# Optimization experiments

Measured on AMD Instinct MI355X. Metric: run time of the kernel, lower is better.

Reference implementation:

```python
import jax, jax.numpy as jnp
import numpy as np

N = 500000   # nodes per graph batch
E = 8000000  # edges per graph batch
B = 4096     # number of graphs
C = 2        # node feature dim
D = 2        # edge feature dim


def setup_inputs() -> dict:
    key = jax.random.key(0)
    ks = jax.random.split(key, 16)
    inp = {
        "x_a": jax.random.normal(ks[0], (N, C), jnp.float32),
        "edge_index_a": jax.random.randint(ks[1], (2, E), 0, N, jnp.int32),
        "edge_attr_a": jax.random.normal(ks[2], (E, D), jnp.float32),
        "batch_a": jnp.sort(jax.random.randint(ks[3], (N,), 0, B, jnp.int32)),
        "x_b": jax.random.normal(ks[4], (N, C), jnp.float32),
        "edge_index_b": jax.random.randint(ks[5], (2, E), 0, N, jnp.int32),
        "edge_attr_b": jax.random.normal(ks[6], (E, D), jnp.float32),
        "batch_b": jnp.sort(jax.random.randint(ks[7], (N,), 0, B, jnp.int32)),
        "targets": jax.random.normal(ks[8], (B,), jnp.float32),
        "num_graphs": B,
        # CGConv params: lin_f, lin_s each Linear(2*C+D=6 -> C)
        "Wf": jax.random.normal(ks[9], (2 * C + D, C), jnp.float32) * 0.4,
        "bf": jnp.zeros((C,), jnp.float32),
        "Ws": jax.random.normal(ks[10], (2 * C + D, C), jnp.float32) * 0.4,
        "bs": jnp.zeros((C,), jnp.float32),
        # l1: Linear(2 -> 3), l2: Linear(6 -> 1)
        "W1": jax.random.normal(ks[11], (C, 3), jnp.float32) * 0.5,
        "b1": jnp.zeros((3,), jnp.float32),
        "W2": jax.random.normal(ks[12], (6, 1), jnp.float32) * 0.4,
        "b2": jnp.zeros((1,), jnp.float32),
    }
    return inp


def cg_conv(x, edge_index, edge_attr, Wf, bf, Ws, bs):
    # PyG CGConv: out_i = x_i + sum_{j->i} sigmoid(lin_f(z)) * softplus(lin_s(z)),
    # z = [x_i, x_j, e_ij]; source_to_target flow => i = edge_index[1].
    src, dst = edge_index[0], edge_index[1]
    z = jnp.concatenate([x[dst], x[src], edge_attr], axis=1)  # [E, 6]
    m = jax.nn.sigmoid(z @ Wf + bf) * jax.nn.softplus(z @ Ws + bs)  # [E, C]
    agg = jax.ops.segment_sum(m, dst, num_segments=x.shape[0])
    return x + agg


def branch(x, edge_index, edge_attr, batch, num_graphs,
           Wf, bf, Ws, bs, W1, b1):
    h = cg_conv(x, edge_index, edge_attr, Wf, bf, Ws, bs)
    h = jax.nn.relu(h @ W1 + b1)  # [N, 3]
    sums = jax.ops.segment_sum(h, batch, num_segments=num_graphs)
    cnts = jax.ops.segment_sum(jnp.ones((h.shape[0],), h.dtype), batch,
                               num_segments=num_graphs)
    return sums / jnp.maximum(cnts, 1.0)[:, None]  # global_mean_pool [B, 3]


def reference(x_a, edge_index_a, edge_attr_a, batch_a,
              x_b, edge_index_b, edge_attr_b, batch_b,
              targets, num_graphs,
              Wf, bf, Ws, bs, W1, b1, W2, b2):
    out_1 = branch(x_a, edge_index_a, edge_attr_a, batch_a, num_graphs,
                   Wf, bf, Ws, bs, W1, b1)
    out_2 = branch(x_b, edge_index_b, edge_attr_b, batch_b, num_graphs,
                   Wf, bf, Ws, bs, W1, b1)
    out = jnp.concatenate([out_1, out_2], axis=1)  # [B, 6]
    out = jax.nn.relu(out @ W2 + b2)               # [B, 1]
    loss = jnp.mean((out[:, 0] - targets) ** 2)
    return out, loss
```

## Files before the change

### kernel.cpp

```cpp
#include <hip/hip_runtime.h>

#define N_NODES 500000
#define N_EDGES 8000000
#define N_GRAPHS 4096

#define NB 128
#define BIN_SHIFT 12
#define BIN_NODES 4096
#define NBINS 123
#define BIN_CAP 66560
#define T_EDGES 2048
#define P1_THREADS 512
#define EPT (T_EDGES / P1_THREADS)
#define P1_GRID ((N_EDGES + T_EDGES - 1) / T_EDGES)
#define K 4
#define P2_GRID (NBINS * K)
#define SLICE_F (BIN_NODES * 2)
#define FXS 131072.0f
#define FXI (1.0f / 131072.0f)
#define M_MAX 250.0f
#define OVF_CAP 8192
#define SGRID ((N_NODES + 255) / 256)

#define OFF_CURS_A   0
#define OFF_CURS_B   512
#define OFF_OVFC_A   1024
#define OFF_OVFC_B   1280
#define ZERO_SMALL   1536
#define OFF_STARTS_A 4096
#define OFF_STARTS_B 20736
#define OFF_MEAN_A   37376
#define OFF_MEAN_B   86528
#define OFF_OVF_A    135680
#define OFF_OVF_B    266752
#define OFF_SCRATCH  397824
#define OFF_BINS     16519680
#define WS_NEED      82014720ull

__device__ __forceinline__ float2 ntload_f2(const float2* p) {
    unsigned long long v = __builtin_nontemporal_load((const unsigned long long*)p);
    float2 r;
    r.x = __uint_as_float((unsigned int)v);
    r.y = __uint_as_float((unsigned int)(v >> 32));
    return r;
}

__global__ __launch_bounds__(512, 8) void p1_kernel(
    const float* __restrict__ x, const int* __restrict__ ei,
    const float* __restrict__ ea,
    const float* __restrict__ Wf, const float* __restrict__ bfv,
    const float* __restrict__ Ws, const float* __restrict__ bsv,
    unsigned long long* __restrict__ bins, unsigned int* __restrict__ cursors,
    unsigned int* __restrict__ ovf_cnt, float4* __restrict__ ovf)
{
    __shared__ unsigned long long sorted[T_EDGES];
    __shared__ unsigned int whist[8][NB];
    __shared__ unsigned int base[NB];
    __shared__ unsigned int cur[NB];
    __shared__ unsigned int gbase[NB];
    __shared__ unsigned int ntot_s;
    unsigned char* binof = (unsigned char*)whist;

    int t = threadIdx.x;
    int wave = t >> 6;
    int ebase = blockIdx.x * T_EDGES;

    for (int i = t; i < 8 * NB; i += P1_THREADS) ((unsigned int*)whist)[i] = 0;
    __syncthreads();

    int d[EPT], s[EPT];
#pragma unroll
    for (int i = 0; i < EPT; ++i) {
        int e = ebase + i * P1_THREADS + t;
        if (e < N_EDGES) {
            d[i] = __builtin_nontemporal_load(ei + N_EDGES + e);
            s[i] = __builtin_nontemporal_load(ei + e);
        } else { d[i] = -1; s[i] = 0; }
        if (d[i] >= 0)
            atomicAdd(&whist[wave][((unsigned)d[i]) >> BIN_SHIFT], 1u);
    }
    __syncthreads();

    unsigned g0 = 0, g1 = 0;
    if (t < 64) {
        unsigned tot0 = 0, tot1 = 0;
#pragma unroll
        for (int w = 0; w < 8; ++w) { tot0 += whist[w][2*t]; tot1 += whist[w][2*t+1]; }
        unsigned pair = tot0 + tot1;
        unsigned v = pair;
#pragma unroll
        for (int off = 1; off < 64; off <<= 1) {
            unsigned u = __shfl_up(v, off);
            if (t >= off) v += u;
        }
        unsigned excl = v - pair;
        base[2*t]   = excl;        cur[2*t]   = excl;
        base[2*t+1] = excl + tot0; cur[2*t+1] = excl + tot0;
        if (t == 63) ntot_s = v;
        g0 = tot0 ? atomicAdd(&cursors[2*t],   tot0) : 0u;
        g1 = tot1 ? atomicAdd(&cursors[2*t+1], tot1) : 0u;
    }
    __syncthreads();

    float2 xdv[EPT], xsv[EPT], eav[EPT];
#pragma unroll
    for (int i = 0; i < EPT; ++i) {
        int e = ebase + i * P1_THREADS + t;
        if (e < N_EDGES) {
            xdv[i] = ((const float2*)x)[d[i]];
            xsv[i] = ((const float2*)x)[s[i]];
            eav[i] = ntload_f2((const float2*)ea + e);
        }
    }

    float wf[12], wsv[12];
#pragma unroll
    for (int i = 0; i < 12; ++i) { wf[i] = Wf[i]; wsv[i] = Ws[i]; }
    float bf0 = bfv[0], bf1 = bfv[1], bs0 = bsv[0], bs1 = bsv[1];

#pragma unroll
    for (int i = 0; i < EPT; ++i) {
        int e = ebase + i * P1_THREADS + t;
        if (e >= N_EDGES) continue;
        int dst = d[i];
        float z0 = xdv[i].x, z1 = xdv[i].y;
        float z2 = xsv[i].x, z3 = xsv[i].y;
        float z4 = eav[i].x, z5 = eav[i].y;

        float f0 = bf0 + z0*wf[0] + z1*wf[2] + z2*wf[4] + z3*wf[6] + z4*wf[8]  + z5*wf[10];
        float f1 = bf1 + z0*wf[1] + z1*wf[3] + z2*wf[5] + z3*wf[7] + z4*wf[9]  + z5*wf[11];
        float s0 = bs0 + z0*wsv[0] + z1*wsv[2] + z2*wsv[4] + z3*wsv[6] + z4*wsv[8]  + z5*wsv[10];
        float s1 = bs1 + z0*wsv[1] + z1*wsv[3] + z2*wsv[5] + z3*wsv[7] + z4*wsv[9]  + z5*wsv[11];

        float m0 = (1.f/(1.f+__expf(-f0))) * (fmaxf(s0,0.f) + __logf(1.f+__expf(-fabsf(s0))));
        float m1 = (1.f/(1.f+__expf(-f1))) * (fmaxf(s1,0.f) + __logf(1.f+__expf(-fabsf(s1))));

        int b = (int)((unsigned)dst >> BIN_SHIFT);
        unsigned slot = atomicAdd(&cur[b], 1u);
        unsigned long long pk = 0ull;
        if (m0 < M_MAX && m1 < M_MAX) {
            unsigned fx0 = __float2uint_rn(m0 * FXS);
            unsigned fx1 = __float2uint_rn(m1 * FXS);
            pk = (unsigned long long)((unsigned)dst & (BIN_NODES - 1))
               | ((unsigned long long)fx0 << 12)
               | ((unsigned long long)fx1 << 37);
        } else {
            unsigned oi = atomicAdd(ovf_cnt, 1u);
            if (oi < OVF_CAP) ovf[oi] = make_float4(__int_as_float(dst), m0, m1, 0.f);
        }
        sorted[slot] = pk;
        binof[slot] = (unsigned char)b;
    }
    if (t < 64) { gbase[2*t] = g0; gbase[2*t+1] = g1; }
    __syncthreads();

    int ntot = (int)ntot_s;
    for (int p = t; p < ntot; p += P1_THREADS) {
        int lo = (int)binof[p];
        unsigned gpos = gbase[lo] + (unsigned)(p - (int)base[lo]);
        unsigned long long v = sorted[p];
        if (gpos < BIN_CAP) {
            __builtin_nontemporal_store(v, &bins[(size_t)lo * BIN_CAP + gpos]);
        } else {
            int local = (int)(v & (BIN_NODES - 1));
            float m0 = (float)((unsigned)((v >> 12) & 0x1FFFFFFu)) * FXI;
            float m1 = (float)((unsigned)((v >> 37) & 0x1FFFFFFu)) * FXI;
            int dst = (lo << BIN_SHIFT) + local;
            unsigned oi = atomicAdd(ovf_cnt, 1u);
            if (oi < OVF_CAP) ovf[oi] = make_float4(__int_as_float(dst), m0, m1, 0.f);
        }
    }
}

__global__ __launch_bounds__(512, 8) void p2_kernel(
    const unsigned long long* __restrict__ bins,
    const unsigned int* __restrict__ cursors,
    float* __restrict__ scratch)
{
    __shared__ float acc[SLICE_F];
    int b = blockIdx.x >> 2;
    int k = blockIdx.x & 3;
    int t = threadIdx.x;
#pragma unroll
    for (int i = t; i < SLICE_F; i += 512) acc[i] = 0.f;
    __syncthreads();

    int n = (int)min(cursors[b], (unsigned)BIN_CAP);
    int s = (n * k) / K, e = (n * (k + 1)) / K;
    const unsigned long long* bp = bins + (size_t)b * BIN_CAP;
    for (int i = s + t; i < e; i += 512) {
        unsigned long long v = __builtin_nontemporal_load(bp + i);
        int local = (int)(v & (BIN_NODES - 1));
        float m0 = (float)((unsigned)((v >> 12) & 0x1FFFFFFu)) * FXI;
        float m1 = (float)((unsigned)((v >> 37) & 0x1FFFFFFu)) * FXI;
        atomicAdd(&acc[local],             m0);
        atomicAdd(&acc[BIN_NODES + local], m1);
    }
    __syncthreads();

    float4* dst = (float4*)(scratch + (size_t)(b * K + k) * SLICE_F);
#pragma unroll
    for (int i = t; i < BIN_NODES / 2; i += 512) {
        float a0 = acc[2*i],             a1 = acc[2*i + 1];
        float b0 = acc[BIN_NODES + 2*i], b1 = acc[BIN_NODES + 2*i + 1];
        dst[i] = make_float4(a0, b0, a1, b1);
    }
}

__global__ __launch_bounds__(256) void ovf_kernel(
    const float4* __restrict__ ovf, const unsigned int* __restrict__ ovf_cnt,
    float* __restrict__ scratch)
{
    int n = (int)min(*ovf_cnt, (unsigned)OVF_CAP);
    for (int i = threadIdx.x; i < n; i += 256) {
        float4 r = ovf[i];
        int dst = __float_as_int(r.x);
        int b = dst >> BIN_SHIFT, local = dst & (BIN_NODES - 1);
        float* p = scratch + (size_t)(b * K) * SLICE_F + 2 * local;
        unsafeAtomicAdd(p,     r.y);
        unsafeAtomicAdd(p + 1, r.z);
    }
}

__global__ __launch_bounds__(256) void starts_kernel(
    const int* __restrict__ ba, const int* __restrict__ bb,
    unsigned int* __restrict__ sa, unsigned int* __restrict__ sb)
{
    int blk = blockIdx.x;
    const int* batch = ba;
    unsigned int* starts = sa;
    if (blk >= SGRID) { blk -= SGRID; batch = bb; starts = sb; }
    int i = blk * 256 + threadIdx.x;
    if (i >= N_NODES) return;
    int b1 = batch[i];
    if (i == 0) {
        for (int g = 0; g <= b1; ++g) starts[g] = 0;
    } else {
        int b0 = batch[i - 1];
        for (int g = b0 + 1; g <= b1; ++g) starts[g] = i;
    }
    if (i == N_NODES - 1) {
        for (int g = b1 + 1; g <= N_GRAPHS; ++g) starts[g] = N_NODES;
    }
}

__global__ __launch_bounds__(256) void pool2_kernel(
    const float* __restrict__ x, const float* __restrict__ scratch,
    const unsigned int* __restrict__ starts,
    const float* __restrict__ W1, const float* __restrict__ b1,
    float* __restrict__ mean_out)
{
    int wave = threadIdx.x >> 6, lane = threadIdx.x & 63;
    int g = blockIdx.x * 4 + wave;

    float w00 = W1[0], w01 = W1[1], w02 = W1[2];
    float w10 = W1[3], w11 = W1[4], w12 = W1[5];
    float c0 = b1[0], c1 = b1[1], c2 = b1[2];

    const float2* sc2 = (const float2*)scratch;
    int s = (int)starts[g], e = (int)starts[g + 1];
    float a0 = 0.f, a1 = 0.f, a2 = 0.f;
    for (int i = s + lane; i < e; i += 64) {
        int b = i >> BIN_SHIFT, local = i & (BIN_NODES - 1);
        size_t f2base = (size_t)(b * K) * BIN_NODES + local;
        float2 g0 = sc2[f2base];
        float2 g1 = sc2[f2base + BIN_NODES];
        float2 g2 = sc2[f2base + 2 * BIN_NODES];
        float2 g3 = sc2[f2base + 3 * BIN_NODES];
        float2 xv = ((const float2*)x)[i];
        float h0 = xv.x + g0.x + g1.x + g2.x + g3.x;
        float h1 = xv.y + g0.y + g1.y + g2.y + g3.y;
        a0 += fmaxf(h0*w00 + h1*w10 + c0, 0.f);
        a1 += fmaxf(h0*w01 + h1*w11 + c1, 0.f);
        a2 += fmaxf(h0*w02 + h1*w12 + c2, 0.f);
    }
#pragma unroll
    for (int off = 32; off; off >>= 1) {
        a0 += __shfl_down(a0, off);
        a1 += __shfl_down(a1, off);
        a2 += __shfl_down(a2, off);
    }
    if (lane == 0) {
        float inv = 1.0f / fmaxf((float)(e - s), 1.0f);
        mean_out[3*(size_t)g]     = a0 * inv;
        mean_out[3*(size_t)g + 1] = a1 * inv;
        mean_out[3*(size_t)g + 2] = a2 * inv;
    }
}

__global__ __launch_bounds__(1024) void final_kernel(
    const float* __restrict__ ma, const float* __restrict__ mb,
    const float* __restrict__ W2, const float* __restrict__ b2,
    const float* __restrict__ targets,
    float* __restrict__ out)
{
    __shared__ float red[1024];
    float w0 = W2[0], w1 = W2[1], w2 = W2[2], w3 = W2[3], w4 = W2[4], w5 = W2[5];
    float bias = b2[0];

    float lsum = 0.f;
    for (int g = threadIdx.x; g < N_GRAPHS; g += 1024) {
        float v = bias
                + ma[3*(size_t)g]*w0 + ma[3*(size_t)g+1]*w1 + ma[3*(size_t)g+2]*w2
                + mb[3*(size_t)g]*w3 + mb[3*(size_t)g+1]*w4 + mb[3*(size_t)g+2]*w5;
        v = fmaxf(v, 0.f);
        out[g] = v;
        float d = v - targets[g];
        lsum += d * d;
    }
    red[threadIdx.x] = lsum;
    __syncthreads();
#pragma unroll
    for (int off = 512; off; off >>= 1) {
        if (threadIdx.x < (unsigned)off) red[threadIdx.x] += red[threadIdx.x + off];
        __syncthreads();
    }
    if (threadIdx.x == 0) out[N_GRAPHS] = red[0] * (1.0f / (float)N_GRAPHS);
}

#define FB_SCALE 4194304.0f
#define FB_INV   2.384185791015625e-07f

__global__ __launch_bounds__(256) void fb_edge_kernel(
    const float* __restrict__ x, const int* __restrict__ ei,
    const float* __restrict__ ea,
    const float* __restrict__ Wf, const float* __restrict__ bfv,
    const float* __restrict__ Ws, const float* __restrict__ bsv,
    unsigned long long* __restrict__ agg)
{
    float wf[12], ws[12];
#pragma unroll
    for (int i = 0; i < 12; ++i) { wf[i] = Wf[i]; ws[i] = Ws[i]; }
    float bf0 = bfv[0], bf1 = bfv[1], bs0 = bsv[0], bs1 = bsv[1];

    int e = blockIdx.x * 256 + threadIdx.x;
    int src = ei[e];
    int dst = ei[N_EDGES + e];
    float2 xd = ((const float2*)x)[dst];
    float2 xs = ((const float2*)x)[src];
    float2 ev = ((const float2*)ea)[e];
    float z0 = xd.x, z1 = xd.y, z2 = xs.x, z3 = xs.y, z4 = ev.x, z5 = ev.y;

    float f0 = bf0 + z0*wf[0] + z1*wf[2] + z2*wf[4] + z3*wf[6] + z4*wf[8]  + z5*wf[10];
    float f1 = bf1 + z0*wf[1] + z1*wf[3] + z2*wf[5] + z3*wf[7] + z4*wf[9]  + z5*wf[11];
    float s0 = bs0 + z0*ws[0] + z1*ws[2] + z2*ws[4] + z3*ws[6] + z4*ws[8]  + z5*ws[10];
    float s1 = bs1 + z0*ws[1] + z1*ws[3] + z2*ws[5] + z3*ws[7] + z4*ws[9]  + z5*ws[11];

    float m0 = (1.f/(1.f+__expf(-f0))) * (fmaxf(s0,0.f) + __logf(1.f+__expf(-fabsf(s0))));
    float m1 = (1.f/(1.f+__expf(-f1))) * (fmaxf(s1,0.f) + __logf(1.f+__expf(-fabsf(s1))));

    unsigned int fx0 = __float2uint_rn(m0 * FB_SCALE);
    unsigned int fx1 = __float2uint_rn(m1 * FB_SCALE);
    atomicAdd(&agg[dst], (unsigned long long)fx0 | ((unsigned long long)fx1 << 32));
}

__global__ __launch_bounds__(64) void fb_pool_kernel(
    const float* __restrict__ x, const unsigned long long* __restrict__ agg,
    const int* __restrict__ batch,
    const float* __restrict__ W1, const float* __restrict__ b1,
    float* __restrict__ mean_out)
{
    int b = blockIdx.x;
    float w00 = W1[0], w01 = W1[1], w02 = W1[2];
    float w10 = W1[3], w11 = W1[4], w12 = W1[5];
    float c0 = b1[0], c1 = b1[1], c2 = b1[2];

    int lo = 0, hi = N_NODES;
    while (lo < hi) { int mid = (lo + hi) >> 1; if (batch[mid] < b) lo = mid + 1; else hi = mid; }
    int seg_s = lo;
    hi = N_NODES;
    while (lo < hi) { int mid = (lo + hi) >> 1; if (batch[mid] < b + 1) lo = mid + 1; else hi = mid; }
    int seg_e = lo;

    float a0 = 0.f, a1 = 0.f, a2 = 0.f;
    for (int i = seg_s + (int)threadIdx.x; i < seg_e; i += 64) {
        unsigned long long v = agg[i];
        float g0 = (float)(unsigned int)(v & 0xffffffffull) * FB_INV;
        float g1 = (float)(unsigned int)(v >> 32) * FB_INV;
        float2 xv = ((const float2*)x)[i];
        float h0 = xv.x + g0, h1 = xv.y + g1;
        a0 += fmaxf(h0*w00 + h1*w10 + c0, 0.f);
        a1 += fmaxf(h0*w01 + h1*w11 + c1, 0.f);
        a2 += fmaxf(h0*w02 + h1*w12 + c2, 0.f);
    }
#pragma unroll
    for (int off = 32; off; off >>= 1) {
        a0 += __shfl_down(a0, off);
        a1 += __shfl_down(a1, off);
        a2 += __shfl_down(a2, off);
    }
    if (threadIdx.x == 0) {
        float inv = 1.0f / fmaxf((float)(seg_e - seg_s), 1.0f);
        mean_out[3*(size_t)b]     = a0 * inv;
        mean_out[3*(size_t)b + 1] = a1 * inv;
        mean_out[3*(size_t)b + 2] = a2 * inv;
    }
}

extern "C" void kernel_launch(void* const* d_in, const int* in_sizes, int n_in,
                              void* d_out, int out_size, void* d_ws, size_t ws_size,
                              hipStream_t stream) {
    const float* x_a     = (const float*)d_in[0];
    const int*   ei_a    = (const int*)  d_in[1];
    const float* ea_a    = (const float*)d_in[2];
    const int*   batch_a = (const int*)  d_in[3];
    const float* x_b     = (const float*)d_in[4];
    const int*   ei_b    = (const int*)  d_in[5];
    const float* ea_b    = (const float*)d_in[6];
    const int*   batch_b = (const int*)  d_in[7];
    const float* targets = (const float*)d_in[8];
    const float* Wf = (const float*)d_in[10];
    const float* bf = (const float*)d_in[11];
    const float* Ws = (const float*)d_in[12];
    const float* bs = (const float*)d_in[13];
    const float* W1 = (const float*)d_in[14];
    const float* b1 = (const float*)d_in[15];
    const float* W2 = (const float*)d_in[16];
    const float* b2 = (const float*)d_in[17];
    float* out = (float*)d_out;
    char* ws = (char*)d_ws;

    if (ws_size >= WS_NEED) {
        unsigned int* curs_a   = (unsigned int*)(ws + OFF_CURS_A);
        unsigned int* curs_b   = (unsigned int*)(ws + OFF_CURS_B);
        unsigned int* ovfc_a   = (unsigned int*)(ws + OFF_OVFC_A);
        unsigned int* ovfc_b   = (unsigned int*)(ws + OFF_OVFC_B);
        unsigned int* starts_a = (unsigned int*)(ws + OFF_STARTS_A);
        unsigned int* starts_b = (unsigned int*)(ws + OFF_STARTS_B);
        float* mean_a = (float*)(ws + OFF_MEAN_A);
        float* mean_b = (float*)(ws + OFF_MEAN_B);
        float4* ovf_a = (float4*)(ws + OFF_OVF_A);
        float4* ovf_b = (float4*)(ws + OFF_OVF_B);
        float* scratch = (float*)(ws + OFF_SCRATCH);
        unsigned long long* bins = (unsigned long long*)(ws + OFF_BINS);

        hipMemsetAsync(ws, 0, ZERO_SMALL, stream);

        starts_kernel<<<2 * SGRID, 256, 0, stream>>>(batch_a, batch_b, starts_a, starts_b);

        p1_kernel<<<P1_GRID, P1_THREADS, 0, stream>>>(x_a, ei_a, ea_a, Wf, bf, Ws, bs,
                                                      bins, curs_a, ovfc_a, ovf_a);
        p2_kernel<<<P2_GRID, 512, 0, stream>>>(bins, curs_a, scratch);
        ovf_kernel<<<1, 256, 0, stream>>>(ovf_a, ovfc_a, scratch);
        pool2_kernel<<<N_GRAPHS / 4, 256, 0, stream>>>(x_a, scratch, starts_a, W1, b1, mean_a);

        p1_kernel<<<P1_GRID, P1_THREADS, 0, stream>>>(x_b, ei_b, ea_b, Wf, bf, Ws, bs,
                                                      bins, curs_b, ovfc_b, ovf_b);
        p2_kernel<<<P2_GRID, 512, 0, stream>>>(bins, curs_b, scratch);
        ovf_kernel<<<1, 256, 0, stream>>>(ovf_b, ovfc_b, scratch);
        pool2_kernel<<<N_GRAPHS / 4, 256, 0, stream>>>(x_b, scratch, starts_b, W1, b1, mean_b);

        final_kernel<<<1, 1024, 0, stream>>>(mean_a, mean_b, W2, b2, targets, out);
    } else {
        unsigned long long* aggu_a = (unsigned long long*)ws;
        unsigned long long* aggu_b = aggu_a + (size_t)N_NODES;
        float* mean_a = (float*)(aggu_b + (size_t)N_NODES);
        float* mean_b = mean_a + 3 * (size_t)N_GRAPHS;

        hipMemsetAsync(ws, 0, 2 * (size_t)N_NODES * sizeof(unsigned long long), stream);
        fb_edge_kernel<<<N_EDGES / 256, 256, 0, stream>>>(x_a, ei_a, ea_a, Wf, bf, Ws, bs, aggu_a);
        fb_edge_kernel<<<N_EDGES / 256, 256, 0, stream>>>(x_b, ei_b, ea_b, Wf, bf, Ws, bs, aggu_b);
        fb_pool_kernel<<<N_GRAPHS, 64, 0, stream>>>(x_a, aggu_a, batch_a, W1, b1, mean_a);
        fb_pool_kernel<<<N_GRAPHS, 64, 0, stream>>>(x_b, aggu_b, batch_b, W1, b1, mean_b);
        final_kernel<<<1, 1024, 0, stream>>>(mean_a, mean_b, W2, b2, targets, out);
    }
}
```

Before: 775.9 us.

## Issue edge gathers early and overlap them with histogram scan in binning kernel

Doubles edges per block to 4096 (8 per thread). The x[dst], x[src] and edge_attr gathers for the first half are now issued before the histogram scan and global cursor atomics, and the second half right after, so memory latency overlaps the scan and barriers. __syncthreads is replaced by a lighter barrier that waits only on LDS counters, and the weights are loaded once as wave-uniform scalars. The larger shared sorted buffer may reduce occupancy, and the two-half split hardcodes EPT=8.

```diff
diff --git a/kernel.cpp b/kernel.cpp
--- a/kernel.cpp
+++ b/kernel.cpp
@@ -9,7 +9,7 @@
 #define BIN_NODES 4096
 #define NBINS 123
 #define BIN_CAP 66560
-#define T_EDGES 2048
+#define T_EDGES 4096
 #define P1_THREADS 512
 #define EPT (T_EDGES / P1_THREADS)
 #define P1_GRID ((N_EDGES + T_EDGES - 1) / T_EDGES)
@@ -45,6 +45,17 @@
     return r;
 }
 
+__device__ __forceinline__ float uniform_f(const float* p) {
+    return __uint_as_float(__builtin_amdgcn_readfirstlane(__float_as_uint(*p)));
+}
+
+#define LIGHT_BARRIER() do {                                   \
+    __builtin_amdgcn_sched_barrier(0);                         \
+    asm volatile("s_waitcnt lgkmcnt(0)" ::: "memory");         \
+    __builtin_amdgcn_s_barrier();                              \
+    __builtin_amdgcn_sched_barrier(0);                         \
+} while (0)
+
 __global__ __launch_bounds__(512, 8) void p1_kernel(
     const float* __restrict__ x, const int* __restrict__ ei,
     const float* __restrict__ ea,
@@ -65,21 +76,40 @@
     int wave = t >> 6;
     int ebase = blockIdx.x * T_EDGES;
 
+    float wf[12], wsv[12];
+#pragma unroll
+    for (int i = 0; i < 12; ++i) { wf[i] = uniform_f(Wf + i); wsv[i] = uniform_f(Ws + i); }
+    float bf0 = uniform_f(bfv + 0), bf1 = uniform_f(bfv + 1);
+    float bs0 = uniform_f(bsv + 0), bs1 = uniform_f(bsv + 1);
+
     for (int i = t; i < 8 * NB; i += P1_THREADS) ((unsigned int*)whist)[i] = 0;
-    __syncthreads();
-
-    int d[EPT], s[EPT];
+    LIGHT_BARRIER();
+
+    int d[EPT], sI[EPT];
 #pragma unroll
     for (int i = 0; i < EPT; ++i) {
         int e = ebase + i * P1_THREADS + t;
         if (e < N_EDGES) {
-            d[i] = __builtin_nontemporal_load(ei + N_EDGES + e);
-            s[i] = __builtin_nontemporal_load(ei + e);
-        } else { d[i] = -1; s[i] = 0; }
+            d[i]  = __builtin_nontemporal_load(ei + N_EDGES + e);
+            sI[i] = __builtin_nontemporal_load(ei + e);
+        } else { d[i] = -1; sI[i] = 0; }
         if (d[i] >= 0)
             atomicAdd(&whist[wave][((unsigned)d[i]) >> BIN_SHIFT], 1u);
     }
-    __syncthreads();
+    LIGHT_BARRIER();
+
+    float2 xdA[4], xsA[4], eaA[4];
+#pragma unroll
+    for (int i = 0; i < 4; ++i) {
+        int e  = ebase + i * P1_THREADS + t;
+        int ec = e < N_EDGES ? e : 0;
+        int dd = d[i] >= 0 ? d[i] : 0;
+        int ss = d[i] >= 0 ? sI[i] : 0;
+        xdA[i] = ((const float2*)x)[dd];
+        xsA[i] = ((const float2*)x)[ss];
+        eaA[i] = ntload_f2((const float2*)ea + ec);
+    }
+    __builtin_amdgcn_sched_barrier(0);
 
     unsigned g0 = 0, g1 = 0;
     if (t < 64) {
@@ -100,56 +130,57 @@
         g0 = tot0 ? atomicAdd(&cursors[2*t],   tot0) : 0u;
         g1 = tot1 ? atomicAdd(&cursors[2*t+1], tot1) : 0u;
     }
-    __syncthreads();
-
-    float2 xdv[EPT], xsv[EPT], eav[EPT];
-#pragma unroll
-    for (int i = 0; i < EPT; ++i) {
-        int e = ebase + i * P1_THREADS + t;
-        if (e < N_EDGES) {
-            xdv[i] = ((const float2*)x)[d[i]];
-            xsv[i] = ((const float2*)x)[s[i]];
-            eav[i] = ntload_f2((const float2*)ea + e);
+    LIGHT_BARRIER();
+
+    float2 xdB[4], xsB[4], eaB[4];
+#pragma unroll
+    for (int i = 0; i < 4; ++i) {
+        int e  = ebase + (i + 4) * P1_THREADS + t;
+        int ec = e < N_EDGES ? e : 0;
+        int dd = d[i+4] >= 0 ? d[i+4] : 0;
+        int ss = d[i+4] >= 0 ? sI[i+4] : 0;
+        xdB[i] = ((const float2*)x)[dd];
+        xsB[i] = ((const float2*)x)[ss];
+        eaB[i] = ntload_f2((const float2*)ea + ec);
+    }
+    __builtin_amdgcn_sched_barrier(0);
+
+#pragma unroll
+    for (int half = 0; half < 2; ++half) {
+#pragma unroll
+        for (int i = 0; i < 4; ++i) {
+            int idx = half * 4 + i;
+            if (d[idx] < 0) continue;
+            int dst = d[idx];
+            float2 xd = half ? xdB[i] : xdA[i];
+            float2 xs = half ? xsB[i] : xsA[i];
+            float2 ev = half ? eaB[i] : eaA[i];
+            float z0 = xd.x, z1 = xd.y, z2 = xs.x, z3 = xs.y, z4 = ev.x, z5 = ev.y;
+
+            float f0 = bf0 + z0*wf[0] + z1*wf[2] + z2*wf[4] + z3*wf[6] + z4*wf[8]  + z5*wf[10];
+            float f1 = bf1 + z0*wf[1] + z1*wf[3] + z2*wf[5] + z3*wf[7] + z4*wf[9]  + z5*wf[11];
+            float s0 = bs0 + z0*wsv[0] + z1*wsv[2] + z2*wsv[4] + z3*wsv[6] + z4*wsv[8]  + z5*wsv[10];
+            float s1 = bs1 + z0*wsv[1] + z1*wsv[3] + z2*wsv[5] + z3*wsv[7] + z4*wsv[9]  + z5*wsv[11];
+
+            float m0 = (1.f/(1.f+__expf(-f0))) * (fmaxf(s0,0.f) + __logf(1.f+__expf(-fabsf(s0))));
+            float m1 = (1.f/(1.f+__expf(-f1))) * (fmaxf(s1,0.f) + __logf(1.f+__expf(-fabsf(s1))));
+
+            int b = (int)((unsigned)dst >> BIN_SHIFT);
+            unsigned slot = atomicAdd(&cur[b], 1u);
+            unsigned long long pk = 0ull;
+            if (m0 < M_MAX && m1 < M_MAX) {
+                unsigned fx0 = __float2uint_rn(m0 * FXS);
+                unsigned fx1 = __float2uint_rn(m1 * FXS);
+                pk = (unsigned long long)((unsigned)dst & (BIN_NODES - 1))
+                   | ((unsigned long long)fx0 << 12)
+                   | ((unsigned long long)fx1 << 37);
+            } else {
+                unsigned oi = atomicAdd(ovf_cnt, 1u);
+                if (oi < OVF_CAP) ovf[oi] = make_float4(__int_as_float(dst), m0, m1, 0.f);
+            }
+            sorted[slot] = pk;
+            binof[slot] = (unsigned char)b;
         }
-    }
-
-    float wf[12], wsv[12];
-#pragma unroll
-    for (int i = 0; i < 12; ++i) { wf[i] = Wf[i]; wsv[i] = Ws[i]; }
-    float bf0 = bfv[0], bf1 = bfv[1], bs0 = bsv[0], bs1 = bsv[1];
-
-#pragma unroll
-    for (int i = 0; i < EPT; ++i) {
-        int e = ebase + i * P1_THREADS + t;
-        if (e >= N_EDGES) continue;
-        int dst = d[i];
-        float z0 = xdv[i].x, z1 = xdv[i].y;
-        float z2 = xsv[i].x, z3 = xsv[i].y;
-        float z4 = eav[i].x, z5 = eav[i].y;
-
-        float f0 = bf0 + z0*wf[0] + z1*wf[2] + z2*wf[4] + z3*wf[6] + z4*wf[8]  + z5*wf[10];
-        float f1 = bf1 + z0*wf[1] + z1*wf[3] + z2*wf[5] + z3*wf[7] + z4*wf[9]  + z5*wf[11];
-        float s0 = bs0 + z0*wsv[0] + z1*wsv[2] + z2*wsv[4] + z3*wsv[6] + z4*wsv[8]  + z5*wsv[10];
-        float s1 = bs1 + z0*wsv[1] + z1*wsv[3] + z2*wsv[5] + z3*wsv[7] + z4*wsv[9]  + z5*wsv[11];
-
-        float m0 = (1.f/(1.f+__expf(-f0))) * (fmaxf(s0,0.f) + __logf(1.f+__expf(-fabsf(s0))));
-        float m1 = (1.f/(1.f+__expf(-f1))) * (fmaxf(s1,0.f) + __logf(1.f+__expf(-fabsf(s1))));
-
-        int b = (int)((unsigned)dst >> BIN_SHIFT);
-        unsigned slot = atomicAdd(&cur[b], 1u);
-        unsigned long long pk = 0ull;
-        if (m0 < M_MAX && m1 < M_MAX) {
-            unsigned fx0 = __float2uint_rn(m0 * FXS);
-            unsigned fx1 = __float2uint_rn(m1 * FXS);
-            pk = (unsigned long long)((unsigned)dst & (BIN_NODES - 1))
-               | ((unsigned long long)fx0 << 12)
-               | ((unsigned long long)fx1 << 37);
-        } else {
-            unsigned oi = atomicAdd(ovf_cnt, 1u);
-            if (oi < OVF_CAP) ovf[oi] = make_float4(__int_as_float(dst), m0, m1, 0.f);
-        }
-        sorted[slot] = pk;
-        binof[slot] = (unsigned char)b;
     }
     if (t < 64) { gbase[2*t] = g0; gbase[2*t+1] = g1; }
     __syncthreads();
```

New measurement: 738.3 us. -4.8%, faster.

## Split linear layer: pack quantized source partials, finish dst terms and activations in bin pass

Applied to the files above, without the earlier changes.

The edge pass now computes only the source-node and edge-attribute contributions to the four pre-activations. It quantizes them to 13-bit fixed point and packs them into the 64-bit binned record, which removes the random gather of x[dst] from the first pass. The second pass reads x for the destination locally within its bin, adds the bias and destination terms, applies sigmoid and softplus, and folds in the overflow records, so the separate overflow kernel is gone. Edges per block are doubled and occupancy bounds are lowered. The trade is extra transcendental work in the bin pass, coarser quantization of the pre-activations with some accuracy risk, and every k==0 block scanning the full overflow list.

```diff
diff --git a/kernel.cpp b/kernel.cpp
--- a/kernel.cpp
+++ b/kernel.cpp
@@ -9,17 +9,18 @@
 #define BIN_NODES 4096
 #define NBINS 123
 #define BIN_CAP 66560
-#define T_EDGES 2048
+#define T_EDGES 4096
 #define P1_THREADS 512
 #define EPT (T_EDGES / P1_THREADS)
 #define P1_GRID ((N_EDGES + T_EDGES - 1) / T_EDGES)
 #define K 4
 #define P2_GRID (NBINS * K)
 #define SLICE_F (BIN_NODES * 2)
-#define FXS 131072.0f
-#define FXI (1.0f / 131072.0f)
-#define M_MAX 250.0f
-#define OVF_CAP 8192
+#define QS 512.0f
+#define QI (1.0f / 512.0f)
+#define P_MAX 7.98f
+#define SENT 0x1FFFu
+#define OVF_CAP 4096
 #define SGRID ((N_NODES + 255) / 256)
 
 #define OFF_CURS_A   0
@@ -45,11 +46,14 @@
     return r;
 }
 
-__global__ __launch_bounds__(512, 8) void p1_kernel(
+__device__ __forceinline__ float uniform_f(const float* p) {
+    return __uint_as_float(__builtin_amdgcn_readfirstlane(__float_as_uint(*p)));
+}
+
+__global__ __launch_bounds__(512, 6) void p1_kernel(
     const float* __restrict__ x, const int* __restrict__ ei,
     const float* __restrict__ ea,
-    const float* __restrict__ Wf, const float* __restrict__ bfv,
-    const float* __restrict__ Ws, const float* __restrict__ bsv,
+    const float* __restrict__ Wf, const float* __restrict__ Ws,
     unsigned long long* __restrict__ bins, unsigned int* __restrict__ cursors,
     unsigned int* __restrict__ ovf_cnt, float4* __restrict__ ovf)
 {
@@ -65,17 +69,21 @@
     int wave = t >> 6;
     int ebase = blockIdx.x * T_EDGES;
 
+    float wf[8], ws[8];
+#pragma unroll
+    for (int i = 0; i < 8; ++i) { wf[i] = uniform_f(Wf + 4 + i); ws[i] = uniform_f(Ws + 4 + i); }
+
     for (int i = t; i < 8 * NB; i += P1_THREADS) ((unsigned int*)whist)[i] = 0;
     __syncthreads();
 
-    int d[EPT], s[EPT];
+    int d[EPT], sI[EPT];
 #pragma unroll
     for (int i = 0; i < EPT; ++i) {
         int e = ebase + i * P1_THREADS + t;
         if (e < N_EDGES) {
-            d[i] = __builtin_nontemporal_load(ei + N_EDGES + e);
-            s[i] = __builtin_nontemporal_load(ei + e);
-        } else { d[i] = -1; s[i] = 0; }
+            d[i]  = __builtin_nontemporal_load(ei + N_EDGES + e);
+            sI[i] = __builtin_nontemporal_load(ei + e);
+        } else { d[i] = -1; sI[i] = 0; }
         if (d[i] >= 0)
             atomicAdd(&whist[wave][((unsigned)d[i]) >> BIN_SHIFT], 1u);
     }
@@ -102,51 +110,48 @@
     }
     __syncthreads();
 
-    float2 xdv[EPT], xsv[EPT], eav[EPT];
+    float2 xs[EPT], ev[EPT];
 #pragma unroll
     for (int i = 0; i < EPT; ++i) {
         int e = ebase + i * P1_THREADS + t;
         if (e < N_EDGES) {
-            xdv[i] = ((const float2*)x)[d[i]];
-            xsv[i] = ((const float2*)x)[s[i]];
-            eav[i] = ntload_f2((const float2*)ea + e);
+            xs[i] = ((const float2*)x)[sI[i]];
+            ev[i] = ntload_f2((const float2*)ea + e);
         }
     }
 
-    float wf[12], wsv[12];
-#pragma unroll
-    for (int i = 0; i < 12; ++i) { wf[i] = Wf[i]; wsv[i] = Ws[i]; }
-    float bf0 = bfv[0], bf1 = bfv[1], bs0 = bsv[0], bs1 = bsv[1];
-
 #pragma unroll
     for (int i = 0; i < EPT; ++i) {
-        int e = ebase + i * P1_THREADS + t;
-        if (e >= N_EDGES) continue;
+        if (d[i] < 0) continue;
         int dst = d[i];
-        float z0 = xdv[i].x, z1 = xdv[i].y;
-        float z2 = xsv[i].x, z3 = xsv[i].y;
-        float z4 = eav[i].x, z5 = eav[i].y;
-
-        float f0 = bf0 + z0*wf[0] + z1*wf[2] + z2*wf[4] + z3*wf[6] + z4*wf[8]  + z5*wf[10];
-        float f1 = bf1 + z0*wf[1] + z1*wf[3] + z2*wf[5] + z3*wf[7] + z4*wf[9]  + z5*wf[11];
-        float s0 = bs0 + z0*wsv[0] + z1*wsv[2] + z2*wsv[4] + z3*wsv[6] + z4*wsv[8]  + z5*wsv[10];
-        float s1 = bs1 + z0*wsv[1] + z1*wsv[3] + z2*wsv[5] + z3*wsv[7] + z4*wsv[9]  + z5*wsv[11];
-
-        float m0 = (1.f/(1.f+__expf(-f0))) * (fmaxf(s0,0.f) + __logf(1.f+__expf(-fabsf(s0))));
-        float m1 = (1.f/(1.f+__expf(-f1))) * (fmaxf(s1,0.f) + __logf(1.f+__expf(-fabsf(s1))));
+        float z2 = xs[i].x, z3 = xs[i].y, z4 = ev[i].x, z5 = ev[i].y;
+        float p0 = z2*wf[0] + z3*wf[2] + z4*wf[4] + z5*wf[6];
+        float p1 = z2*wf[1] + z3*wf[3] + z4*wf[5] + z5*wf[7];
+        float p2 = z2*ws[0] + z3*ws[2] + z4*ws[4] + z5*ws[6];
+        float p3 = z2*ws[1] + z3*ws[3] + z4*ws[5] + z5*ws[7];
 
         int b = (int)((unsigned)dst >> BIN_SHIFT);
+        unsigned local = (unsigned)dst & (BIN_NODES - 1);
         unsigned slot = atomicAdd(&cur[b], 1u);
-        unsigned long long pk = 0ull;
-        if (m0 < M_MAX && m1 < M_MAX) {
-            unsigned fx0 = __float2uint_rn(m0 * FXS);
-            unsigned fx1 = __float2uint_rn(m1 * FXS);
-            pk = (unsigned long long)((unsigned)dst & (BIN_NODES - 1))
-               | ((unsigned long long)fx0 << 12)
-               | ((unsigned long long)fx1 << 37);
+        float mx = fmaxf(fmaxf(fabsf(p0), fabsf(p1)), fmaxf(fabsf(p2), fabsf(p3)));
+        unsigned long long pk;
+        if (mx < P_MAX) {
+            unsigned q0 = __float2uint_rn(p0 * QS + 4096.0f);
+            unsigned q1 = __float2uint_rn(p1 * QS + 4096.0f);
+            unsigned q2 = __float2uint_rn(p2 * QS + 4096.0f);
+            unsigned q3 = __float2uint_rn(p3 * QS + 4096.0f);
+            pk = (unsigned long long)local
+               | ((unsigned long long)q0 << 12)
+               | ((unsigned long long)q1 << 25)
+               | ((unsigned long long)q2 << 38)
+               | ((unsigned long long)q3 << 51);
         } else {
+            pk = (unsigned long long)local | ((unsigned long long)SENT << 12);
             unsigned oi = atomicAdd(ovf_cnt, 1u);
-            if (oi < OVF_CAP) ovf[oi] = make_float4(__int_as_float(dst), m0, m1, 0.f);
+            if (oi < OVF_CAP) {
+                ovf[2*oi]   = make_float4(__int_as_float(dst), p0, p1, p2);
+                ovf[2*oi+1] = make_float4(p3, 0.f, 0.f, 0.f);
+            }
         }
         sorted[slot] = pk;
         binof[slot] = (unsigned char)b;
@@ -162,12 +167,20 @@
         if (gpos < BIN_CAP) {
             __builtin_nontemporal_store(v, &bins[(size_t)lo * BIN_CAP + gpos]);
         } else {
-            int local = (int)(v & (BIN_NODES - 1));
-            float m0 = (float)((unsigned)((v >> 12) & 0x1FFFFFFu)) * FXI;
-            float m1 = (float)((unsigned)((v >> 37) & 0x1FFFFFFu)) * FXI;
-            int dst = (lo << BIN_SHIFT) + local;
-            unsigned oi = atomicAdd(ovf_cnt, 1u);
-            if (oi < OVF_CAP) ovf[oi] = make_float4(__int_as_float(dst), m0, m1, 0.f);
+            unsigned q0 = (unsigned)(v >> 12) & 0x1FFFu;
+            if (q0 != SENT) {
+                int local = (int)(v & (BIN_NODES - 1));
+                int dst = (lo << BIN_SHIFT) + local;
+                float p0 = (float)q0 * QI - 8.f;
+                float p1 = (float)((unsigned)(v >> 25) & 0x1FFFu) * QI - 8.f;
+                float p2 = (float)((unsigned)(v >> 38) & 0x1FFFu) * QI - 8.f;
+                float p3 = (float)((unsigned)(v >> 51) & 0x1FFFu) * QI - 8.f;
+                unsigned oi = atomicAdd(ovf_cnt, 1u);
+                if (oi < OVF_CAP) {
+                    ovf[2*oi]   = make_float4(__int_as_float(dst), p0, p1, p2);
+                    ovf[2*oi+1] = make_float4(p3, 0.f, 0.f, 0.f);
+                }
+            }
         }
     }
 }
@@ -175,50 +188,75 @@
 __global__ __launch_bounds__(512, 8) void p2_kernel(
     const unsigned long long* __restrict__ bins,
     const unsigned int* __restrict__ cursors,
+    const float* __restrict__ x,
+    const float* __restrict__ Wf, const float* __restrict__ bfv,
+    const float* __restrict__ Ws, const float* __restrict__ bsv,
+    const float4* __restrict__ ovf, const unsigned int* __restrict__ ovf_cnt,
     float* __restrict__ scratch)
 {
     __shared__ float acc[SLICE_F];
     int b = blockIdx.x >> 2;
     int k = blockIdx.x & 3;
     int t = threadIdx.x;
+
+    float wf0 = uniform_f(Wf+0), wf1 = uniform_f(Wf+1), wf2 = uniform_f(Wf+2), wf3 = uniform_f(Wf+3);
+    float ws0 = uniform_f(Ws+0), ws1 = uniform_f(Ws+1), ws2 = uniform_f(Ws+2), ws3 = uniform_f(Ws+3);
+    float bf0 = uniform_f(bfv+0), bf1 = uniform_f(bfv+1);
+    float bs0 = uniform_f(bsv+0), bs1 = uniform_f(bsv+1);
+    float bf0m = bf0 - 8.f, bf1m = bf1 - 8.f, bs0m = bs0 - 8.f, bs1m = bs1 - 8.f;
+
 #pragma unroll
     for (int i = t; i < SLICE_F; i += 512) acc[i] = 0.f;
     __syncthreads();
 
+    const float2* xb = (const float2*)x + ((size_t)b << BIN_SHIFT);
     int n = (int)min(cursors[b], (unsigned)BIN_CAP);
     int s = (n * k) / K, e = (n * (k + 1)) / K;
     const unsigned long long* bp = bins + (size_t)b * BIN_CAP;
     for (int i = s + t; i < e; i += 512) {
         unsigned long long v = __builtin_nontemporal_load(bp + i);
+        unsigned q0 = (unsigned)(v >> 12) & 0x1FFFu;
         int local = (int)(v & (BIN_NODES - 1));
-        float m0 = (float)((unsigned)((v >> 12) & 0x1FFFFFFu)) * FXI;
-        float m1 = (float)((unsigned)((v >> 37) & 0x1FFFFFFu)) * FXI;
-        atomicAdd(&acc[local],             m0);
-        atomicAdd(&acc[BIN_NODES + local], m1);
+        float2 xd = xb[local];
+        if (q0 != SENT) {
+            float f0 = bf0m + (float)q0 * QI                            + xd.x*wf0 + xd.y*wf2;
+            float f1 = bf1m + (float)((unsigned)(v >> 25) & 0x1FFFu)*QI + xd.x*wf1 + xd.y*wf3;
+            float s0 = bs0m + (float)((unsigned)(v >> 38) & 0x1FFFu)*QI + xd.x*ws0 + xd.y*ws2;
+            float s1 = bs1m + (float)((unsigned)(v >> 51) & 0x1FFFu)*QI + xd.x*ws1 + xd.y*ws3;
+            float m0 = (1.f/(1.f+__expf(-f0))) * (fmaxf(s0,0.f) + __logf(1.f+__expf(-fabsf(s0))));
+            float m1 = (1.f/(1.f+__expf(-f1))) * (fmaxf(s1,0.f) + __logf(1.f+__expf(-fabsf(s1))));
+            atomicAdd(&acc[local],             m0);
+            atomicAdd(&acc[BIN_NODES + local], m1);
+        }
+    }
+
+    if (k == 0) {
+        int no = (int)min(*ovf_cnt, (unsigned)OVF_CAP);
+        for (int i = t; i < no; i += 512) {
+            float4 r0 = ovf[2*i];
+            float4 r1 = ovf[2*i+1];
+            int dst = __float_as_int(r0.x);
+            if ((dst >> BIN_SHIFT) == b) {
+                int local = dst & (BIN_NODES - 1);
+                float2 xd = xb[local];
+                float f0 = bf0 + r0.y + xd.x*wf0 + xd.y*wf2;
+                float f1 = bf1 + r0.z + xd.x*wf1 + xd.y*wf3;
+                float s0 = bs0 + r0.w + xd.x*ws0 + xd.y*ws2;
+                float s1 = bs1 + r1.x + xd.x*ws1 + xd.y*ws3;
+                float m0 = (1.f/(1.f+__expf(-f0))) * (fmaxf(s0,0.f) + __logf(1.f+__expf(-fabsf(s0))));
+                float m1 = (1.f/(1.f+__expf(-f1))) * (fmaxf(s1,0.f) + __logf(1.f+__expf(-fabsf(s1))));
+                atomicAdd(&acc[local],             m0);
+                atomicAdd(&acc[BIN_NODES + local], m1);
+            }
+        }
     }
     __syncthreads();
 
     float4* dst = (float4*)(scratch + (size_t)(b * K + k) * SLICE_F);
 #pragma unroll
     for (int i = t; i < BIN_NODES / 2; i += 512) {
-        float a0 = acc[2*i],             a1 = acc[2*i + 1];
-        float b0 = acc[BIN_NODES + 2*i], b1 = acc[BIN_NODES + 2*i + 1];
-        dst[i] = make_float4(a0, b0, a1, b1);
-    }
-}
-
-__global__ __launch_bounds__(256) void ovf_kernel(
-    const float4* __restrict__ ovf, const unsigned int* __restrict__ ovf_cnt,
-    float* __restrict__ scratch)
-{
-    int n = (int)min(*ovf_cnt, (unsigned)OVF_CAP);
-    for (int i = threadIdx.x; i < n; i += 256) {
-        float4 r = ovf[i];
-        int dst = __float_as_int(r.x);
-        int b = dst >> BIN_SHIFT, local = dst & (BIN_NODES - 1);
-        float* p = scratch + (size_t)(b * K) * SLICE_F + 2 * local;
-        unsafeAtomicAdd(p,     r.y);
-        unsafeAtomicAdd(p + 1, r.z);
+        dst[i] = make_float4(acc[2*i], acc[BIN_NODES + 2*i],
+                             acc[2*i + 1], acc[BIN_NODES + 2*i + 1]);
     }
 }
 
@@ -438,16 +476,16 @@
 
         starts_kernel<<<2 * SGRID, 256, 0, stream>>>(batch_a, batch_b, starts_a, starts_b);
 
-        p1_kernel<<<P1_GRID, P1_THREADS, 0, stream>>>(x_a, ei_a, ea_a, Wf, bf, Ws, bs,
+        p1_kernel<<<P1_GRID, P1_THREADS, 0, stream>>>(x_a, ei_a, ea_a, Wf, Ws,
                                                       bins, curs_a, ovfc_a, ovf_a);
-        p2_kernel<<<P2_GRID, 512, 0, stream>>>(bins, curs_a, scratch);
-        ovf_kernel<<<1, 256, 0, stream>>>(ovf_a, ovfc_a, scratch);
+        p2_kernel<<<P2_GRID, 512, 0, stream>>>(bins, curs_a, x_a, Wf, bf, Ws, bs,
+                                               ovf_a, ovfc_a, scratch);
         pool2_kernel<<<N_GRAPHS / 4, 256, 0, stream>>>(x_a, scratch, starts_a, W1, b1, mean_a);
 
-        p1_kernel<<<P1_GRID, P1_THREADS, 0, stream>>>(x_b, ei_b, ea_b, Wf, bf, Ws, bs,
+        p1_kernel<<<P1_GRID, P1_THREADS, 0, stream>>>(x_b, ei_b, ea_b, Wf, Ws,
                                                       bins, curs_b, ovfc_b, ovf_b);
-        p2_kernel<<<P2_GRID, 512, 0, stream>>>(bins, curs_b, scratch);
-        ovf_kernel<<<1, 256, 0, stream>>>(ovf_b, ovfc_b, scratch);
+        p2_kernel<<<P2_GRID, 512, 0, stream>>>(bins, curs_b, x_b, Wf, bf, Ws, bs,
+                                               ovf_b, ovfc_b, scratch);
         pool2_kernel<<<N_GRAPHS / 4, 256, 0, stream>>>(x_b, scratch, starts_b, W1, b1, mean_b);
 
         final_kernel<<<1, 1024, 0, stream>>>(mean_a, mean_b, W2, b2, targets, out);
```

Result: faster. 655.9 us (-15.5%).
